# Optimization experiments

Hardware: AMD Instinct MI355X
Metric: run time of the kernel (lower is better)

The kernel has to match this reference:

```python
import jax, jax.numpy as jnp
import numpy as np
import math

N_HEADS = 16
D_MODEL = 1024
D_FF = 4096
MAX_REL = 32  # max_relative_position
LN_EPS = 1e-5


def _layernorm(x, g, b):
    m = jnp.mean(x, axis=-1, keepdims=True)
    v = jnp.var(x, axis=-1, keepdims=True)
    return (x - m) * jax.lax.rsqrt(v + LN_EPS) * g + b


def setup_inputs() -> dict:
    key = jax.random.key(0)
    ks = jax.random.split(key, 12)
    D, F = D_MODEL, D_FF
    gain = 1.0 / math.sqrt(2.0)
    xav = lambda k, o, i, g=1.0: jax.random.uniform(k, (o, i), jnp.float32, -1.0, 1.0) * (g * math.sqrt(6.0 / (o + i)))
    return {
        "x": jax.random.normal(ks[0], (2, 2048, D), jnp.float32),
        "wq": xav(ks[1], D, D, gain),
        "wk": xav(ks[2], D, D, gain),
        "wv": xav(ks[3], D, D, gain),
        "wo": xav(ks[4], D, D, gain),
        "wo_b": jnp.zeros((D,), jnp.float32),
        "rel_tab": jax.random.normal(ks[5], (2 * MAX_REL - 1, N_HEADS), jnp.float32) * 0.02,
        "ln1_g": jnp.ones((D,), jnp.float32),
        "ln1_b": jnp.zeros((D,), jnp.float32),
        "ln2_g": jnp.ones((D,), jnp.float32),
        "ln2_b": jnp.zeros((D,), jnp.float32),
        "w1": xav(ks[6], F, D),
        "b1": jnp.zeros((F,), jnp.float32),
        "w2": xav(ks[7], D, F),
        "b2": jnp.zeros((D,), jnp.float32),
    }


def reference(x, wq, wk, wv, wo, wo_b, rel_tab, ln1_g, ln1_b, ln2_g, ln2_b, w1, b1, w2, b2):
    B, S, D = x.shape
    H = N_HEADS
    dk = D // H

    def proj(w):  # torch Linear: x @ w.T, then split heads -> [B,H,S,dk]
        return (x @ w.T).reshape(B, S, H, dk).transpose(0, 2, 1, 3)

    q, k, v = proj(wq), proj(wk), proj(wv)

    # Rotary embeddings (per-head dim), exact interleave-to-block formula from source
    t = jnp.arange(S, dtype=jnp.float32)
    inv_freq = 1.0 / (10000.0 ** (jnp.arange(0, dk, 2, dtype=jnp.float32) / dk))
    freqs = t[:, None] * inv_freq[None, :]  # [S, dk/2]
    cos, sin = jnp.cos(freqs), jnp.sin(freqs)

    def rope(z):
        z1, z2 = z[..., ::2], z[..., 1::2]  # [B,H,S,dk/2]
        return jnp.concatenate([z1 * cos - z2 * sin, z1 * sin + z2 * cos], axis=-1)

    q, k = rope(q), rope(k)

    # Manual attention with learned relative-position bias
    scores = jnp.einsum("bhqd,bhkd->bhqk", q, k) / math.sqrt(dk)
    rel = jnp.arange(S)[:, None] - jnp.arange(S)[None, :]
    rel = jnp.clip(rel, -(MAX_REL - 1), MAX_REL - 1) + (MAX_REL - 1)
    bias = rel_tab[rel]  # [S,S,H]
    scores = scores + jnp.transpose(bias, (2, 0, 1))[None]  # [1,H,S,S]
    attn = jax.nn.softmax(scores, axis=-1)
    o = jnp.einsum("bhqk,bhkd->bhqd", attn, v).transpose(0, 2, 1, 3).reshape(B, S, D)
    o = o @ wo.T + wo_b

    # Post-norm residual block
    h = _layernorm(x + o, ln1_g, ln1_b)
    f = jax.nn.gelu(h @ w1.T + b1, approximate=False) @ w2.T + b2
    return _layernorm(h + f, ln2_g, ln2_b)
```

## Files before the change

### kernel.cpp

```cpp
#include <hip/hip_runtime.h>
#include <stdint.h>

#define MB (1ull << 20)
typedef unsigned short u16;
typedef __attribute__((ext_vector_type(8))) short bf16x8;
typedef __attribute__((ext_vector_type(4))) float f32x4;

__device__ __forceinline__ float b2f(u16 u) {
  union { unsigned int i; float f; } c; c.i = ((unsigned int)u) << 16; return c.f;
}
__device__ __forceinline__ u16 f2b(float f) {
  union { float f; unsigned int i; } c; c.f = f;
  unsigned int r = c.i + 0x7fffu + ((c.i >> 16) & 1u);
  return (u16)(r >> 16);
}
__device__ __forceinline__ void gload16(const void* g, void* l) {
  __builtin_amdgcn_global_load_lds(
      (const __attribute__((address_space(1))) void*)g,
      (__attribute__((address_space(3))) void*)l, 16, 0, 0);
}

__global__ __launch_bounds__(256) void f2b_all(
    const float* __restrict__ x, const float* __restrict__ wq, const float* __restrict__ wk,
    const float* __restrict__ wv, const float* __restrict__ wo, const float* __restrict__ w1,
    const float* __restrict__ w2,
    u16* __restrict__ xb, u16* __restrict__ wqkvb, u16* __restrict__ wob,
    u16* __restrict__ w1b, u16* __restrict__ w2b)
{
  int bid = blockIdx.x;
  const float* src; u16* dst;
  if (bid < 4096)       { src = x;  dst = xb; }
  else if (bid < 5120)  { src = wq; dst = wqkvb;           bid -= 4096; }
  else if (bid < 6144)  { src = wk; dst = wqkvb + 1048576; bid -= 5120; }
  else if (bid < 7168)  { src = wv; dst = wqkvb + 2097152; bid -= 6144; }
  else if (bid < 8192)  { src = wo; dst = wob;             bid -= 7168; }
  else if (bid < 12288) { src = w1; dst = w1b;             bid -= 8192; }
  else                  { src = w2; dst = w2b;             bid -= 12288; }
  int i = (bid * 256 + threadIdx.x) * 4;
  float4 v = *(const float4*)(src + i);
  uint2 ov;
  ov.x = (unsigned)f2b(v.x) | ((unsigned)f2b(v.y) << 16);
  ov.y = (unsigned)f2b(v.z) | ((unsigned)f2b(v.w) << 16);
  *(uint2*)(dst + i) = ov;
}

__global__ __launch_bounds__(256) void rope_tab_kernel(float2* __restrict__ tab) {
  int idx = blockIdx.x * 256 + threadIdx.x;
  int s = idx >> 5, j = idx & 31;
  float inv = exp2f(-(float)j * (13.287712379549449f / 32.0f));
  float sn, cs;
  sincosf((float)s * inv, &sn, &cs);
  tab[idx] = make_float2(cs, sn);
}

template<int EPI, int BM>
__global__ __launch_bounds__(256) void gemm_bt(
    const u16* __restrict__ A, const u16* __restrict__ B,
    u16* __restrict__ C, const float* __restrict__ bias,
    int M, int N, int K)
{
  constexpr int MT = BM / 32;
  __shared__ __align__(16) u16 As[BM * 64];
  __shared__ __align__(16) u16 Bs[128 * 64];
  const int tid = threadIdx.x;
  const int lane = tid & 63, wave = tid >> 6;
  const int lr = lane & 15, lg = lane >> 4;
  const int wm = wave >> 1, wn = wave & 1;

  const int nwg = gridDim.x * gridDim.y;
  const int id = blockIdx.y * gridDim.x + blockIdx.x;
  const int nid = (id & 7) * (nwg >> 3) + (id >> 3);
  const int bx = nid % gridDim.x, by = nid / gridDim.x;

  const int srow = tid >> 3;
  const int scsw = ((tid & 7) * 8) ^ ((srow & 7) << 3);
  const size_t abase = (size_t)(by * BM + srow) * K + scsw;
  const size_t bbase = (size_t)(bx * 128 + srow) * K + scsw;

  int aoff[MT][2], boff[4][2];
  #pragma unroll
  for (int mt = 0; mt < MT; mt++) {
    int row = wm * (BM / 2) + mt * 16 + lr;
    #pragma unroll
    for (int kk = 0; kk < 2; kk++)
      aoff[mt][kk] = row * 64 + ((kk * 32 + lg * 8) ^ ((row & 7) << 3));
  }
  #pragma unroll
  for (int nt = 0; nt < 4; nt++) {
    int row = wn * 64 + nt * 16 + lr;
    #pragma unroll
    for (int kk = 0; kk < 2; kk++)
      boff[nt][kk] = row * 64 + ((kk * 32 + lg * 8) ^ ((row & 7) << 3));
  }

  f32x4 acc[MT][4];
  #pragma unroll
  for (int i = 0; i < MT; i++)
    #pragma unroll
    for (int j = 0; j < 4; j++) acc[i][j] = (f32x4){0.f, 0.f, 0.f, 0.f};

  for (int k0 = 0; k0 < K; k0 += 64) {
    __syncthreads();
    #pragma unroll
    for (int h = 0; h < MT; h++)
      gload16(A + abase + (size_t)(h * 32) * K + k0, &As[h * 2048 + tid * 8]);
    #pragma unroll
    for (int h = 0; h < 4; h++)
      gload16(B + bbase + (size_t)(h * 32) * K + k0, &Bs[h * 2048 + tid * 8]);
    __syncthreads();
    #pragma unroll
    for (int kk = 0; kk < 2; kk++) {
      bf16x8 af[MT], bfr[4];
      #pragma unroll
      for (int mt = 0; mt < MT; mt++) af[mt] = *(const bf16x8*)&As[aoff[mt][kk]];
      #pragma unroll
      for (int nt = 0; nt < 4; nt++) bfr[nt] = *(const bf16x8*)&Bs[boff[nt][kk]];
      #pragma unroll
      for (int mt = 0; mt < MT; mt++)
        #pragma unroll
        for (int nt = 0; nt < 4; nt++)
          acc[mt][nt] = __builtin_amdgcn_mfma_f32_16x16x32_bf16(af[mt], bfr[nt], acc[mt][nt], 0, 0, 0);
    }
  }

  #pragma unroll
  for (int mt = 0; mt < MT; mt++)
    #pragma unroll
    for (int nt = 0; nt < 4; nt++) {
      const int row = by * BM + wm * (BM / 2) + mt * 16 + lg * 4;
      const int col = bx * 128 + wn * 64 + nt * 16 + lr;
      const float bv = (EPI >= 1) ? bias[col] : 0.f;
      #pragma unroll
      for (int r = 0; r < 4; r++) {
        float x = acc[mt][nt][r] + bv;
        if (EPI == 2) x = 0.5f * x * (1.f + erff(x * 0.70710678118654752f));
        C[(size_t)(row + r) * N + col] = f2b(x);
      }
    }
}

#define MFMA16(BASE, BF)                                                       \
  __builtin_amdgcn_s_setprio(1);                                               \
  _Pragma("unroll")                                                            \
  for (int mt = 0; mt < 4; mt++)                                               \
    _Pragma("unroll")                                                          \
    for (int nt = 0; nt < 4; nt++)                                             \
      acc[(BASE) + mt][nt] = __builtin_amdgcn_mfma_f32_16x16x32_bf16(          \
          af[mt], BF[nt], acc[(BASE) + mt][nt], 0, 0, 0);                      \
  __builtin_amdgcn_s_setprio(0);

#define SA2(bb, eta, kb)                                                             \
  gload16(Ab + ((size_t)(eta) * 128) * K + (kb), &As[bb][eta][tid * 8]);             \
  gload16(Ab + ((size_t)(eta) * 128 + 64) * K + (kb), &As[bb][eta][4096 + tid * 8]);
#define SB2(bb, eta, kb)                                                             \
  gload16(Bb + ((size_t)(eta) * 128) * K + (kb), &Bs[bb][eta][tid * 8]);             \
  gload16(Bb + ((size_t)(eta) * 128 + 64) * K + (kb), &Bs[bb][eta][4096 + tid * 8]);

#define SBAR asm volatile("s_barrier" ::: "memory")

template<int EPI>
__global__ __launch_bounds__(512) void gemm256(
    const u16* __restrict__ A, const u16* __restrict__ B,
    u16* __restrict__ C, const float* __restrict__ bias,
    int M, int N, int K)
{
  __shared__ __align__(16) u16 As[2][2][8192];
  __shared__ __align__(16) u16 Bs[2][2][8192];
  const int tid = threadIdx.x;
  const int lane = tid & 63, wave = tid >> 6;
  const int lr = lane & 15, lg = lane >> 4;
  const int wm = wave >> 2, wn = wave & 3;

  const int nwg = gridDim.x * gridDim.y;
  const int id = blockIdx.y * gridDim.x + blockIdx.x;
  const int nid = (id & 7) * (nwg >> 3) + (id >> 3);
  const int bx = nid % gridDim.x, by = nid / gridDim.x;

  const int srow = tid >> 3;
  const int scsw = ((tid & 7) * 8) ^ ((srow & 7) << 3);
  const u16* Ab = A + (size_t)(by * 256 + srow) * K + scsw;
  const u16* Bb = B + (size_t)(bx * 256 + srow) * K + scsw;

  int aoff[2][2][4], boff[2][4];
  #pragma unroll
  for (int mh = 0; mh < 2; mh++)
    #pragma unroll
    for (int kk = 0; kk < 2; kk++)
      #pragma unroll
      for (int mt = 0; mt < 4; mt++) {
        int row = mh * 64 + mt * 16 + lr;
        aoff[mh][kk][mt] = row * 64 + ((kk * 32 + lg * 8) ^ ((lr & 7) << 3));
      }
  #pragma unroll
  for (int kk = 0; kk < 2; kk++)
    #pragma unroll
    for (int nt = 0; nt < 4; nt++) {
      int row = (wn & 1) * 64 + nt * 16 + lr;
      boff[kk][nt] = row * 64 + ((kk * 32 + lg * 8) ^ ((lr & 7) << 3));
    }

  f32x4 acc[8][4];
  #pragma unroll
  for (int i = 0; i < 8; i++)
    #pragma unroll
    for (int j = 0; j < 4; j++) acc[i][j] = (f32x4){0.f, 0.f, 0.f, 0.f};

  const int NT = K >> 6;

  SB2(0, 0, 0) SB2(0, 1, 0) SA2(0, 0, 0) SA2(0, 1, 0)

  for (int t = 0; t < NT; ++t) {
    const int c = t & 1, n = c ^ 1;
    const size_t kb = (size_t)(t + 1) * 64;
    const bool st = (t + 1 < NT);
    const u16* Ac = As[c][wm];
    const u16* Bc = Bs[c][wn >> 1];
    bf16x8 b0[4], b1[4], af[4];

    asm volatile("s_waitcnt vmcnt(0)" ::: "memory");
    SBAR;
    #pragma unroll
    for (int nt = 0; nt < 4; nt++) b0[nt] = *(const bf16x8*)&Bc[boff[0][nt]];
    #pragma unroll
    for (int mt = 0; mt < 4; mt++) af[mt] = *(const bf16x8*)&Ac[aoff[0][0][mt]];
    if (st) { SB2(n, 0, kb) }
    MFMA16(0, b0)
    SBAR;
    #pragma unroll
    for (int nt = 0; nt < 4; nt++) b1[nt] = *(const bf16x8*)&Bc[boff[1][nt]];
    #pragma unroll
    for (int mt = 0; mt < 4; mt++) af[mt] = *(const bf16x8*)&Ac[aoff[0][1][mt]];
    if (st) { SA2(n, 0, kb) }
    SBAR;
    MFMA16(0, b1)
    SBAR;
    #pragma unroll
    for (int mt = 0; mt < 4; mt++) af[mt] = *(const bf16x8*)&Ac[aoff[1][0][mt]];
    if (st) { SB2(n, 1, kb) }
    SBAR;
    MFMA16(4, b0)
    SBAR;
    #pragma unroll
    for (int mt = 0; mt < 4; mt++) af[mt] = *(const bf16x8*)&Ac[aoff[1][1][mt]];
    if (st) { SA2(n, 1, kb) }
    SBAR;
    MFMA16(4, b1)
    SBAR;
  }

  #pragma unroll
  for (int m8 = 0; m8 < 8; m8++)
    #pragma unroll
    for (int nt = 0; nt < 4; nt++) {
      const int row = by * 256 + wm * 128 + m8 * 16 + lg * 4;
      const int col = bx * 256 + wn * 64 + nt * 16 + lr;
      const float bv = (EPI >= 1) ? bias[col] : 0.f;
      #pragma unroll
      for (int r = 0; r < 4; r++) {
        float x = acc[m8][nt][r] + bv;
        if (EPI == 2) x = 0.5f * x * (1.f + erff(x * 0.70710678118654752f));
        C[(size_t)(row + r) * N + col] = f2b(x);
      }
    }
}

__global__ __launch_bounds__(256) void rope_kernel(
    const u16* __restrict__ qp, const u16* __restrict__ kp, int stride,
    const float2* __restrict__ tab, u16* __restrict__ qr, u16* __restrict__ kr)
{
  const int gid = blockIdx.x * 4 + (threadIdx.x >> 6);
  const int lane = threadIdx.x & 63;
  const int s = gid & 2047;
  const int bh = gid >> 11;
  const int h = bh & 15, b = bh >> 4;
  const int j = lane & 31;
  float2 t = tab[s * 32 + j];
  const float cs = t.x, sn = t.y;
  const size_t base = (size_t)(b * 2048 + s) * stride + h * 64;
  unsigned int qv = *(const unsigned int*)(qp + base + 2 * j);
  unsigned int kv = *(const unsigned int*)(kp + base + 2 * j);
  float q1 = b2f((u16)qv), q2 = b2f((u16)(qv >> 16));
  float k1 = b2f((u16)kv), k2 = b2f((u16)(kv >> 16));
  float qo = (lane < 32) ? (q1 * cs - q2 * sn) : (q1 * sn + q2 * cs);
  float ko = (lane < 32) ? (k1 * cs - k2 * sn) : (k1 * sn + k2 * cs);
  qr[(size_t)gid * 64 + lane] = f2b(qo * 0.18033688011112042f);
  kr[(size_t)gid * 64 + lane] = f2b(ko);
}

__global__ __launch_bounds__(256) void vtrans_kernel(
    const u16* __restrict__ vp, int stride, u16* __restrict__ vT)
{
  __shared__ u16 t[64][65];
  const int sc = blockIdx.x & 31;
  const int bh = blockIdx.x >> 5;
  const int h = bh & 15, b = bh >> 4;
  const int tid = threadIdx.x;
  #pragma unroll
  for (int i = 0; i < 16; i++) {
    int idx = i * 256 + tid;
    int sl = idx >> 6, d = idx & 63;
    t[sl][d] = vp[(size_t)(b * 2048 + sc * 64 + sl) * stride + h * 64 + d];
  }
  __syncthreads();
  #pragma unroll
  for (int i = 0; i < 16; i++) {
    int idx = i * 256 + tid;
    int d = idx >> 6, sl = idx & 63;
    vT[((size_t)bh * 64 + d) * 2048 + sc * 64 + sl] = t[sl][d];
  }
}

__global__ __launch_bounds__(256) void attn_kernel(
    const u16* __restrict__ qr, const u16* __restrict__ kr,
    const u16* __restrict__ vT, const float* __restrict__ rel_tab,
    u16* __restrict__ o)
{
  __shared__ __align__(16) u16 Ks[2][64 * 64];
  __shared__ __align__(16) u16 Vs[2][64 * 64];
  __shared__ float bias_s[64];

  const int tid = threadIdx.x;
  const int lane = tid & 63, wave = tid >> 6;
  const int lr = lane & 15, lg = lane >> 4;

  const int id = blockIdx.x;
  const int nid = (id & 7) * 128 + (id >> 3);
  const int bh = nid >> 5, qc = nid & 31;
  const int h = bh & 15, b = bh >> 4;
  const int q0 = qc * 64 + wave * 16;

  if (tid < 63) bias_s[tid] = rel_tab[tid * 16 + h] * 1.4426950408889634f;

  const u16* qb = qr + (size_t)bh * 2048 * 64;
  const u16* kb = kr + (size_t)bh * 2048 * 64;
  const u16* vb = vT + (size_t)bh * 64 * 2048;

  bf16x8 qf[2];
  qf[0] = *(const bf16x8*)(qb + (size_t)(q0 + lr) * 64 + lg * 8);
  qf[1] = *(const bf16x8*)(qb + (size_t)(q0 + lr) * 64 + 32 + lg * 8);

  const int srow = tid >> 3;
  const int scsw = ((tid & 7) * 8) ^ ((srow & 7) << 3);

  int koff[4][2];
  #pragma unroll
  for (int nt = 0; nt < 4; nt++)
    #pragma unroll
    for (int ks = 0; ks < 2; ks++)
      koff[nt][ks] = (nt * 16 + lr) * 64 + ((ks * 32 + lg * 8) ^ ((lr & 7) << 3));

  #pragma unroll
  for (int hh = 0; hh < 2; hh++) {
    gload16(kb + (size_t)(hh * 32 + srow) * 64 + scsw, &Ks[0][hh * 2048 + tid * 8]);
    gload16(vb + (size_t)(hh * 32 + srow) * 2048 + scsw, &Vs[0][hh * 2048 + tid * 8]);
  }

  float mrow = -1e30f;
  f32x4 lvec = (f32x4){0.f, 0.f, 0.f, 0.f};
  f32x4 oacc[4];
  #pragma unroll
  for (int nt = 0; nt < 4; nt++) oacc[nt] = (f32x4){0.f, 0.f, 0.f, 0.f};

  const int idx_lo = 4 * (lr + 16 * ((lg & 1) * 2));
  const int idx_hi = idx_lo + 64;
  const bool hiSel = (lg >= 2);

  int cur = 0;
  for (int kc = 0; kc < 32; kc++) {
    const int k0 = kc * 64;
    __syncthreads();
    if (kc < 31) {
      const int kn = k0 + 64;
      #pragma unroll
      for (int hh = 0; hh < 2; hh++) {
        gload16(kb + (size_t)(kn + hh * 32 + srow) * 64 + scsw, &Ks[cur ^ 1][hh * 2048 + tid * 8]);
        gload16(vb + (size_t)(hh * 32 + srow) * 2048 + kn + scsw, &Vs[cur ^ 1][hh * 2048 + tid * 8]);
      }
    }
    const u16* Kc = Ks[cur];
    const u16* Vc = Vs[cur];

    f32x4 sacc[4];
    #pragma unroll
    for (int nt = 0; nt < 4; nt++) sacc[nt] = (f32x4){0.f, 0.f, 0.f, 0.f};
    __builtin_amdgcn_s_setprio(1);
    #pragma unroll
    for (int ks = 0; ks < 2; ks++)
      #pragma unroll
      for (int nt = 0; nt < 4; nt++) {
        bf16x8 kf = *(const bf16x8*)&Kc[koff[nt][ks]];
        sacc[nt] = __builtin_amdgcn_mfma_f32_16x16x32_bf16(kf, qf[ks], sacc[nt], 0, 0, 0);
      }
    __builtin_amdgcn_s_setprio(0);

    f32x4 pvv[4];
    const int dmin = q0 - k0 - 63, dmax = q0 + 15 - k0;
    if (dmin >= 31 || dmax <= -31) {
      const float c = bias_s[dmin >= 31 ? 62 : 0];
      f32x4 m4;
      #pragma unroll
      for (int i = 0; i < 4; i++)
        m4[i] = fmaxf(fmaxf(sacc[0][i], sacc[1][i]), fmaxf(sacc[2][i], sacc[3][i]));
      float rm = fmaxf(fmaxf(m4[0], m4[1]), fmaxf(m4[2], m4[3])) + c;
      rm = fmaxf(rm, __shfl_xor(rm, 16));
      rm = fmaxf(rm, __shfl_xor(rm, 32));
      if (!__all(rm <= mrow + 11.5f)) {
        float mnew = fmaxf(mrow, rm);
        float sc = exp2f(mrow - mnew);
        lvec *= sc;
        #pragma unroll
        for (int nt = 0; nt < 4; nt++) oacc[nt] *= sc;
        mrow = mnew;
      }
      const float off = c - mrow;
      #pragma unroll
      for (int nt = 0; nt < 4; nt++) pvv[nt] = sacc[nt] + off;
    } else {
      #pragma unroll
      for (int nt = 0; nt < 4; nt++)
        #pragma unroll
        for (int r = 0; r < 4; r++) {
          int d = (q0 + lr) - (k0 + nt * 16 + lg * 4 + r);
          d = d < -31 ? -31 : (d > 31 ? 31 : d);
          pvv[nt][r] = sacc[nt][r] + bias_s[d + 31];
        }
      f32x4 m4;
      #pragma unroll
      for (int i = 0; i < 4; i++)
        m4[i] = fmaxf(fmaxf(pvv[0][i], pvv[1][i]), fmaxf(pvv[2][i], pvv[3][i]));
      float rm = fmaxf(fmaxf(m4[0], m4[1]), fmaxf(m4[2], m4[3]));
      rm = fmaxf(rm, __shfl_xor(rm, 16));
      rm = fmaxf(rm, __shfl_xor(rm, 32));
      if (!__all(rm <= mrow + 11.5f)) {
        float mnew = fmaxf(mrow, rm);
        float sc = exp2f(mrow - mnew);
        lvec *= sc;
        #pragma unroll
        for (int nt = 0; nt < 4; nt++) oacc[nt] *= sc;
        mrow = mnew;
      }
      #pragma unroll
      for (int nt = 0; nt < 4; nt++) pvv[nt] = pvv[nt] - mrow;
    }

    unsigned int pk[4][2];
    #pragma unroll
    for (int nt = 0; nt < 4; nt++) {
      f32x4 p;
      #pragma unroll
      for (int i = 0; i < 4; i++) p[i] = exp2f(pvv[nt][i]);
      lvec += p;
      unsigned int pr0, pr1;
      asm("v_cvt_pk_bf16_f32 %0, %1, %2" : "=v"(pr0) : "v"(p[0]), "v"(p[1]));
      asm("v_cvt_pk_bf16_f32 %0, %1, %2" : "=v"(pr1) : "v"(p[2]), "v"(p[3]));
      pk[nt][0] = pr0;
      pk[nt][1] = pr1;
    }

    __builtin_amdgcn_s_setprio(1);
    #pragma unroll
    for (int ks = 0; ks < 2; ks++) {
      int w0a = __builtin_amdgcn_ds_bpermute(idx_lo, (int)pk[ks * 2][0]);
      int w0b = __builtin_amdgcn_ds_bpermute(idx_lo, (int)pk[ks * 2 + 1][0]);
      int w1a = __builtin_amdgcn_ds_bpermute(idx_lo, (int)pk[ks * 2][1]);
      int w1b = __builtin_amdgcn_ds_bpermute(idx_lo, (int)pk[ks * 2 + 1][1]);
      int w2a = __builtin_amdgcn_ds_bpermute(idx_hi, (int)pk[ks * 2][0]);
      int w2b = __builtin_amdgcn_ds_bpermute(idx_hi, (int)pk[ks * 2 + 1][0]);
      int w3a = __builtin_amdgcn_ds_bpermute(idx_hi, (int)pk[ks * 2][1]);
      int w3b = __builtin_amdgcn_ds_bpermute(idx_hi, (int)pk[ks * 2 + 1][1]);
      int4 bw;
      bw.x = hiSel ? w0b : w0a;
      bw.y = hiSel ? w1b : w1a;
      bw.z = hiSel ? w2b : w2a;
      bw.w = hiSel ? w3b : w3a;
      bf16x8 pf = *(bf16x8*)&bw;
      #pragma unroll
      for (int nt = 0; nt < 4; nt++) {
        bf16x8 vf = *(const bf16x8*)&Vc[koff[nt][ks]];
        oacc[nt] = __builtin_amdgcn_mfma_f32_16x16x32_bf16(vf, pf, oacc[nt], 0, 0, 0);
      }
    }
    __builtin_amdgcn_s_setprio(0);
    cur ^= 1;
  }

  float lpart = (lvec[0] + lvec[1]) + (lvec[2] + lvec[3]);
  lpart += __shfl_xor(lpart, 16);
  lpart += __shfl_xor(lpart, 32);
  const float inv = 1.0f / lpart;
  const size_t obase = (size_t)(b * 2048 + q0 + lr) * 1024 + h * 64;
  #pragma unroll
  for (int nt = 0; nt < 4; nt++) {
    uint2 st;
    st.x = (unsigned)f2b(oacc[nt][0] * inv) | ((unsigned)f2b(oacc[nt][1] * inv) << 16);
    st.y = (unsigned)f2b(oacc[nt][2] * inv) | ((unsigned)f2b(oacc[nt][3] * inv) << 16);
    *(uint2*)(o + obase + nt * 16 + lg * 4) = st;
  }
}

__global__ __launch_bounds__(256) void ln1_kernel(
    const float* __restrict__ x, const u16* __restrict__ ao,
    const float* __restrict__ g, const float* __restrict__ bta,
    u16* __restrict__ hb)
{
  const int row = blockIdx.x, tid = threadIdx.x;
  const int wave = tid >> 6, lane = tid & 63;
  const int c = tid * 4;
  float4 xv = *(const float4*)(x + (size_t)row * 1024 + c);
  uint2 av = *(const uint2*)(ao + (size_t)row * 1024 + c);
  float v0 = xv.x + b2f((u16)av.x);
  float v1 = xv.y + b2f((u16)(av.x >> 16));
  float v2 = xv.z + b2f((u16)av.y);
  float v3 = xv.w + b2f((u16)(av.y >> 16));
  float s = (v0 + v1) + (v2 + v3);
  float s2 = (v0 * v0 + v1 * v1) + (v2 * v2 + v3 * v3);
  #pragma unroll
  for (int off = 32; off >= 1; off >>= 1) { s += __shfl_down(s, off); s2 += __shfl_down(s2, off); }
  __shared__ float rs[4], rs2[4];
  if (lane == 0) { rs[wave] = s; rs2[wave] = s2; }
  __syncthreads();
  s = rs[0] + rs[1] + rs[2] + rs[3];
  s2 = rs2[0] + rs2[1] + rs2[2] + rs2[3];
  float mean = s * (1.f / 1024.f);
  float var = s2 * (1.f / 1024.f) - mean * mean;
  float inv = rsqrtf(var + 1e-5f);
  float4 gv = *(const float4*)(g + c);
  float4 bv = *(const float4*)(bta + c);
  uint2 ov;
  ov.x = (unsigned)f2b((v0 - mean) * inv * gv.x + bv.x) |
         ((unsigned)f2b((v1 - mean) * inv * gv.y + bv.y) << 16);
  ov.y = (unsigned)f2b((v2 - mean) * inv * gv.z + bv.z) |
         ((unsigned)f2b((v3 - mean) * inv * gv.w + bv.w) << 16);
  *(uint2*)(hb + (size_t)row * 1024 + c) = ov;
}

__global__ __launch_bounds__(256) void ln2_kernel(
    const u16* __restrict__ hb, const u16* __restrict__ fb,
    const float* __restrict__ g, const float* __restrict__ bta,
    float* __restrict__ out)
{
  const int row = blockIdx.x, tid = threadIdx.x;
  const int wave = tid >> 6, lane = tid & 63;
  const int c = tid * 4;
  uint2 hv = *(const uint2*)(hb + (size_t)row * 1024 + c);
  uint2 fv = *(const uint2*)(fb + (size_t)row * 1024 + c);
  float v0 = b2f((u16)hv.x) + b2f((u16)fv.x);
  float v1 = b2f((u16)(hv.x >> 16)) + b2f((u16)(fv.x >> 16));
  float v2 = b2f((u16)hv.y) + b2f((u16)fv.y);
  float v3 = b2f((u16)(hv.y >> 16)) + b2f((u16)(fv.y >> 16));
  float s = (v0 + v1) + (v2 + v3);
  float s2 = (v0 * v0 + v1 * v1) + (v2 * v2 + v3 * v3);
  #pragma unroll
  for (int off = 32; off >= 1; off >>= 1) { s += __shfl_down(s, off); s2 += __shfl_down(s2, off); }
  __shared__ float rs[4], rs2[4];
  if (lane == 0) { rs[wave] = s; rs2[wave] = s2; }
  __syncthreads();
  s = rs[0] + rs[1] + rs[2] + rs[3];
  s2 = rs2[0] + rs2[1] + rs2[2] + rs2[3];
  float mean = s * (1.f / 1024.f);
  float var = s2 * (1.f / 1024.f) - mean * mean;
  float inv = rsqrtf(var + 1e-5f);
  float4 gv = *(const float4*)(g + c);
  float4 bv = *(const float4*)(bta + c);
  float4 ov;
  ov.x = (v0 - mean) * inv * gv.x + bv.x;
  ov.y = (v1 - mean) * inv * gv.y + bv.y;
  ov.z = (v2 - mean) * inv * gv.z + bv.z;
  ov.w = (v3 - mean) * inv * gv.w + bv.w;
  *(float4*)(out + (size_t)row * 1024 + c) = ov;
}

extern "C" void kernel_launch(void* const* d_in, const int* in_sizes, int n_in,
                              void* d_out, int out_size, void* d_ws, size_t ws_size,
                              hipStream_t stream)
{
  const float* x    = (const float*)d_in[0];
  const float* wq   = (const float*)d_in[1];
  const float* wk   = (const float*)d_in[2];
  const float* wv   = (const float*)d_in[3];
  const float* wo   = (const float*)d_in[4];
  const float* wo_b = (const float*)d_in[5];
  const float* rel  = (const float*)d_in[6];
  const float* ln1g = (const float*)d_in[7];
  const float* ln1b = (const float*)d_in[8];
  const float* ln2g = (const float*)d_in[9];
  const float* ln2b = (const float*)d_in[10];
  const float* w1   = (const float*)d_in[11];
  const float* b1   = (const float*)d_in[12];
  const float* w2   = (const float*)d_in[13];
  const float* b2   = (const float*)d_in[14];
  float* out = (float*)d_out;
  char* w = (char*)d_ws;

  if (ws_size < (size_t)90 * MB) return;

  u16* xb    = (u16*)(w + 0 * MB);
  u16* wqkvb = (u16*)(w + 8 * MB);
  u16* wob   = (u16*)(w + 14 * MB);
  u16* w1b   = (u16*)(w + 16 * MB);
  u16* w2b   = (u16*)(w + 24 * MB);
  u16* qkv   = (u16*)(w + 32 * MB);
  u16* ob    = (u16*)(w + 32 * MB);
  u16* ao    = (u16*)(w + 40 * MB);
  u16* hb    = (u16*)(w + 48 * MB);
  u16* qrb   = (u16*)(w + 56 * MB);
  u16* krb   = (u16*)(w + 64 * MB);
  u16* vTb   = (u16*)(w + 72 * MB);
  u16* gb    = (u16*)(w + 56 * MB);
  u16* fb    = (u16*)(w + 0 * MB);
  float2* tab = (float2*)(w + 88 * MB);

  const int M = 4096, D = 1024, F = 4096;

  rope_tab_kernel<<<dim3(256), 256, 0, stream>>>(tab);
  f2b_all<<<dim3(16384), 256, 0, stream>>>(x, wq, wk, wv, wo, w1, w2,
                                           xb, wqkvb, wob, w1b, w2b);

  gemm256<0><<<dim3(3 * D / 256, M / 256), 512, 0, stream>>>(xb, wqkvb, qkv, nullptr, M, 3 * D, D);

  rope_kernel<<<dim3(16384), 256, 0, stream>>>(qkv, qkv + 1024, 3 * D, tab, qrb, krb);
  vtrans_kernel<<<dim3(1024), 256, 0, stream>>>(qkv + 2048, 3 * D, vTb);

  attn_kernel<<<dim3(1024), 256, 0, stream>>>(qrb, krb, vTb, rel, ob);

  gemm_bt<1, 64><<<dim3(D / 128, M / 64), 256, 0, stream>>>(ob, wob, ao, wo_b, M, D, D);

  ln1_kernel<<<dim3(M), 256, 0, stream>>>(x, ao, ln1g, ln1b, hb);

  gemm256<2><<<dim3(F / 256, M / 256), 512, 0, stream>>>(hb, w1b, gb, b1, M, F, D);

  gemm_bt<1, 64><<<dim3(D / 128, M / 64), 256, 0, stream>>>(gb, w2b, fb, b2, M, D, F);

  ln2_kernel<<<dim3(M), 256, 0, stream>>>(hb, fb, ln2g, ln2b, out);
}
```

Before: 289.6 us.

## Split-K the FFN down-projection and load V directly into registers in attention

The second FFN GEMM (K=4096) becomes a split-K kernel with two K halves. Each half writes bf16 partials to separate buffers, and ln2 sums them and adds the bias. This doubles the workgroup count on a GEMM that had only 512 blocks, at the cost of extra partial writes and reads plus an extra bf16 rounding. Separately, the attention kernel drops the V LDS staging and loads V fragments straight from global memory into registers each iteration. That saves LDS and barrier traffic but exposes global-load latency to the PV MFMAs.

```diff
diff --git a/kernel.cpp b/kernel.cpp
--- a/kernel.cpp
+++ b/kernel.cpp
@@ -136,6 +136,90 @@
         if (EPI == 2) x = 0.5f * x * (1.f + erff(x * 0.70710678118654752f));
         C[(size_t)(row + r) * N + col] = f2b(x);
       }
+    }
+}
+
+__global__ __launch_bounds__(256) void gemm_ks(
+    const u16* __restrict__ A, const u16* __restrict__ B,
+    u16* __restrict__ C, int M, int N, int K)
+{
+  constexpr int BM = 64, MT = 2;
+  __shared__ __align__(16) u16 As[BM * 64];
+  __shared__ __align__(16) u16 Bs[128 * 64];
+  const int tid = threadIdx.x;
+  const int lane = tid & 63, wave = tid >> 6;
+  const int lr = lane & 15, lg = lane >> 4;
+  const int wm = wave >> 1, wn = wave & 1;
+
+  const int nwg = gridDim.x * gridDim.y;
+  const int id = blockIdx.y * gridDim.x + blockIdx.x;
+  const int nid = (id & 7) * (nwg >> 3) + (id >> 3);
+  const int bx = nid % gridDim.x, byk = nid / gridDim.x;
+  const int kslice = byk & 1, by = byk >> 1;
+  const int Kh = K >> 1;
+  const int kofs = kslice * Kh;
+  u16* Cs = C + (size_t)kslice * M * N;
+
+  const int srow = tid >> 3;
+  const int scsw = ((tid & 7) * 8) ^ ((srow & 7) << 3);
+  const size_t abase = (size_t)(by * BM + srow) * K + kofs + scsw;
+  const size_t bbase = (size_t)(bx * 128 + srow) * K + kofs + scsw;
+
+  int aoff[MT][2], boff[4][2];
+  #pragma unroll
+  for (int mt = 0; mt < MT; mt++) {
+    int row = wm * (BM / 2) + mt * 16 + lr;
+    #pragma unroll
+    for (int kk = 0; kk < 2; kk++)
+      aoff[mt][kk] = row * 64 + ((kk * 32 + lg * 8) ^ ((row & 7) << 3));
+  }
+  #pragma unroll
+  for (int nt = 0; nt < 4; nt++) {
+    int row = wn * 64 + nt * 16 + lr;
+    #pragma unroll
+    for (int kk = 0; kk < 2; kk++)
+      boff[nt][kk] = row * 64 + ((kk * 32 + lg * 8) ^ ((row & 7) << 3));
+  }
+
+  f32x4 acc[MT][4];
+  #pragma unroll
+  for (int i = 0; i < MT; i++)
+    #pragma unroll
+    for (int j = 0; j < 4; j++) acc[i][j] = (f32x4){0.f, 0.f, 0.f, 0.f};
+
+  for (int k0 = 0; k0 < Kh; k0 += 64) {
+    __syncthreads();
+    #pragma unroll
+    for (int h = 0; h < MT; h++)
+      gload16(A + abase + (size_t)(h * 32) * K + k0, &As[h * 2048 + tid * 8]);
+    #pragma unroll
+    for (int h = 0; h < 4; h++)
+      gload16(B + bbase + (size_t)(h * 32) * K + k0, &Bs[h * 2048 + tid * 8]);
+    __syncthreads();
+    #pragma unroll
+    for (int kk = 0; kk < 2; kk++) {
+      bf16x8 af[MT], bfr[4];
+      #pragma unroll
+      for (int mt = 0; mt < MT; mt++) af[mt] = *(const bf16x8*)&As[aoff[mt][kk]];
+      #pragma unroll
+      for (int nt = 0; nt < 4; nt++) bfr[nt] = *(const bf16x8*)&Bs[boff[nt][kk]];
+      #pragma unroll
+      for (int mt = 0; mt < MT; mt++)
+        #pragma unroll
+        for (int nt = 0; nt < 4; nt++)
+          acc[mt][nt] = __builtin_amdgcn_mfma_f32_16x16x32_bf16(af[mt], bfr[nt], acc[mt][nt], 0, 0, 0);
+    }
+  }
+
+  #pragma unroll
+  for (int mt = 0; mt < MT; mt++)
+    #pragma unroll
+    for (int nt = 0; nt < 4; nt++) {
+      const int row = by * BM + wm * (BM / 2) + mt * 16 + lg * 4;
+      const int col = bx * 128 + wn * 64 + nt * 16 + lr;
+      #pragma unroll
+      for (int r = 0; r < 4; r++)
+        Cs[(size_t)(row + r) * N + col] = f2b(acc[mt][nt][r]);
     }
 }
 
@@ -316,7 +400,6 @@
     u16* __restrict__ o)
 {
   __shared__ __align__(16) u16 Ks[2][64 * 64];
-  __shared__ __align__(16) u16 Vs[2][64 * 64];
   __shared__ float bias_s[64];
 
   const int tid = threadIdx.x;
@@ -349,11 +432,16 @@
     for (int ks = 0; ks < 2; ks++)
       koff[nt][ks] = (nt * 16 + lr) * 64 + ((ks * 32 + lg * 8) ^ ((lr & 7) << 3));
 
-  #pragma unroll
-  for (int hh = 0; hh < 2; hh++) {
+  size_t voff[2][4];
+  #pragma unroll
+  for (int ks = 0; ks < 2; ks++)
+    #pragma unroll
+    for (int nt = 0; nt < 4; nt++)
+      voff[ks][nt] = (size_t)(nt * 16 + lr) * 2048 + ks * 32 + lg * 8;
+
+  #pragma unroll
+  for (int hh = 0; hh < 2; hh++)
     gload16(kb + (size_t)(hh * 32 + srow) * 64 + scsw, &Ks[0][hh * 2048 + tid * 8]);
-    gload16(vb + (size_t)(hh * 32 + srow) * 2048 + scsw, &Vs[0][hh * 2048 + tid * 8]);
-  }
 
   float mrow = -1e30f;
   f32x4 lvec = (f32x4){0.f, 0.f, 0.f, 0.f};
@@ -369,16 +457,19 @@
   for (int kc = 0; kc < 32; kc++) {
     const int k0 = kc * 64;
     __syncthreads();
+    bf16x8 vreg[2][4];
+    #pragma unroll
+    for (int ks = 0; ks < 2; ks++)
+      #pragma unroll
+      for (int nt = 0; nt < 4; nt++)
+        vreg[ks][nt] = *(const bf16x8*)(vb + voff[ks][nt] + k0);
     if (kc < 31) {
       const int kn = k0 + 64;
       #pragma unroll
-      for (int hh = 0; hh < 2; hh++) {
+      for (int hh = 0; hh < 2; hh++)
         gload16(kb + (size_t)(kn + hh * 32 + srow) * 64 + scsw, &Ks[cur ^ 1][hh * 2048 + tid * 8]);
-        gload16(vb + (size_t)(hh * 32 + srow) * 2048 + kn + scsw, &Vs[cur ^ 1][hh * 2048 + tid * 8]);
-      }
     }
     const u16* Kc = Ks[cur];
-    const u16* Vc = Vs[cur];
 
     f32x4 sacc[4];
     #pragma unroll
@@ -475,10 +566,8 @@
       bw.w = hiSel ? w3b : w3a;
       bf16x8 pf = *(bf16x8*)&bw;
       #pragma unroll
-      for (int nt = 0; nt < 4; nt++) {
-        bf16x8 vf = *(const bf16x8*)&Vc[koff[nt][ks]];
-        oacc[nt] = __builtin_amdgcn_mfma_f32_16x16x32_bf16(vf, pf, oacc[nt], 0, 0, 0);
-      }
+      for (int nt = 0; nt < 4; nt++)
+        oacc[nt] = __builtin_amdgcn_mfma_f32_16x16x32_bf16(vreg[ks][nt], pf, oacc[nt], 0, 0, 0);
     }
     __builtin_amdgcn_s_setprio(0);
     cur ^= 1;
@@ -535,7 +624,8 @@
 }
 
 __global__ __launch_bounds__(256) void ln2_kernel(
-    const u16* __restrict__ hb, const u16* __restrict__ fb,
+    const u16* __restrict__ hb, const u16* __restrict__ fb0,
+    const u16* __restrict__ fb1, const float* __restrict__ b2,
     const float* __restrict__ g, const float* __restrict__ bta,
     float* __restrict__ out)
 {
@@ -543,11 +633,13 @@
   const int wave = tid >> 6, lane = tid & 63;
   const int c = tid * 4;
   uint2 hv = *(const uint2*)(hb + (size_t)row * 1024 + c);
-  uint2 fv = *(const uint2*)(fb + (size_t)row * 1024 + c);
-  float v0 = b2f((u16)hv.x) + b2f((u16)fv.x);
-  float v1 = b2f((u16)(hv.x >> 16)) + b2f((u16)(fv.x >> 16));
-  float v2 = b2f((u16)hv.y) + b2f((u16)fv.y);
-  float v3 = b2f((u16)(hv.y >> 16)) + b2f((u16)(fv.y >> 16));
+  uint2 f0 = *(const uint2*)(fb0 + (size_t)row * 1024 + c);
+  uint2 f1 = *(const uint2*)(fb1 + (size_t)row * 1024 + c);
+  float4 b2v = *(const float4*)(b2 + c);
+  float v0 = b2f((u16)hv.x) + b2f((u16)f0.x) + b2f((u16)f1.x) + b2v.x;
+  float v1 = b2f((u16)(hv.x >> 16)) + b2f((u16)(f0.x >> 16)) + b2f((u16)(f1.x >> 16)) + b2v.y;
+  float v2 = b2f((u16)hv.y) + b2f((u16)f0.y) + b2f((u16)f1.y) + b2v.z;
+  float v3 = b2f((u16)(hv.y >> 16)) + b2f((u16)(f0.y >> 16)) + b2f((u16)(f1.y >> 16)) + b2v.w;
   float s = (v0 + v1) + (v2 + v3);
   float s2 = (v0 * v0 + v1 * v1) + (v2 * v2 + v3 * v3);
   #pragma unroll
@@ -607,7 +699,7 @@
   u16* krb   = (u16*)(w + 64 * MB);
   u16* vTb   = (u16*)(w + 72 * MB);
   u16* gb    = (u16*)(w + 56 * MB);
-  u16* fb    = (u16*)(w + 0 * MB);
+  u16* fb01  = (u16*)(w + 0 * MB);
   float2* tab = (float2*)(w + 88 * MB);
 
   const int M = 4096, D = 1024, F = 4096;
@@ -629,7 +721,8 @@
 
   gemm256<2><<<dim3(F / 256, M / 256), 512, 0, stream>>>(hb, w1b, gb, b1, M, F, D);
 
-  gemm_bt<1, 64><<<dim3(D / 128, M / 64), 256, 0, stream>>>(gb, w2b, fb, b2, M, D, F);
-
-  ln2_kernel<<<dim3(M), 256, 0, stream>>>(hb, fb, ln2g, ln2b, out);
-}
+  gemm_ks<<<dim3(D / 128, (M / 64) * 2), 256, 0, stream>>>(gb, w2b, fb01, M, D, F);
+
+  ln2_kernel<<<dim3(M), 256, 0, stream>>>(hb, fb01, fb01 + (size_t)M * D, b2,
+                                          ln2g, ln2b, out);
+}
```

After: 351.2 us. 1.21x slower.
